# Kernel optimization log

Measured on AMD Instinct MI355X. Metric: run time of the kernel, lower is better.

Reference implementation:

```python
import jax, jax.numpy as jnp
import numpy as np
from jax import lax

B, C1, C2, OUT, H, W = 8, 256, 128, 256, 64, 64
MID = max(C1, C2)
D = max(MID // 8, 4)

def conv1x1(x, w, b=None):
    # x: [B,C,H,W], w: [O,C]
    y = jnp.einsum('bchw,oc->bohw', x, w)
    if b is not None:
        y = y + b[None, :, None, None]
    return y

def dwconv3x3(x, w, b):
    # depthwise 3x3, padding=1; w: [C,1,3,3]
    y = lax.conv_general_dilated(x, w, (1, 1), 'SAME',
                                 dimension_numbers=('NCHW', 'OIHW', 'NCHW'),
                                 feature_group_count=x.shape[1])
    return y + b[None, :, None, None]

def setup_inputs() -> dict:
    key = jax.random.key(0)
    ks = jax.random.split(key, 16)
    def w1x1(k, o, i):
        return jax.random.normal(k, (o, i), jnp.float32) * np.sqrt(2.0 / o)
    def wdw(k, c):
        return jax.random.normal(k, (c, 1, 3, 3), jnp.float32) * np.sqrt(2.0 / (9 * c))
    z = lambda c: jnp.zeros((c,), jnp.float32)
    return {
        'x1': jax.random.normal(ks[0], (B, C1, H, W), jnp.float32),
        'x2': jax.random.normal(ks[1], (B, C2, H, W), jnp.float32),
        'conv_r_w': w1x1(ks[2], MID, C1), 'conv_r_b': z(MID),
        'conv_n_w': w1x1(ks[3], MID, C2), 'conv_n_b': z(MID),
        'mlp_w1': w1x1(ks[4], D, MID),
        'mlp_w2': w1x1(ks[5], 2 * MID, D),
        'pq_w': w1x1(ks[6], MID, MID), 'pq_b': z(MID),
        'dq_w': wdw(ks[7], MID), 'dq_b': z(MID),
        'pk_w': w1x1(ks[8], MID, MID), 'pk_b': z(MID),
        'dk_w': wdw(ks[9], MID), 'dk_b': z(MID),
        'pv_w': w1x1(ks[10], MID, MID), 'pv_b': z(MID),
        'dv_w': wdw(ks[11], MID), 'dv_b': z(MID),
        'out_w': w1x1(ks[12], OUT, MID), 'out_b': z(OUT),
        'alpha': jnp.float32(1.0),
        'lambd': jnp.float32(0.5),
        'beta': jnp.float32(0.5),
    }

def reference(x1, x2, conv_r_w, conv_r_b, conv_n_w, conv_n_b, mlp_w1, mlp_w2,
              pq_w, pq_b, dq_w, dq_b, pk_w, pk_b, dk_w, dk_b,
              pv_w, pv_b, dv_w, dv_b, out_w, out_b, alpha, lambd, beta):
    FR = conv1x1(x1, conv_r_w, conv_r_b)          # [B,C,H,W]
    FN = conv1x1(x2, conv_n_w, conv_n_b)          # [B,C,H,W]
    stack = jnp.stack([FR, FN], axis=1)           # [B,2,C,H,W]
    feats_sum = FR + FN
    pooled = feats_sum.mean(axis=(2, 3))          # [B,C] (adaptive avg pool 1x1)
    h = jax.nn.relu(jnp.einsum('bc,dc->bd', pooled, mlp_w1))
    a = jnp.einsum('bd,ed->be', h, mlp_w2).reshape(B, 2, MID)
    attn = jax.nn.softmax(a, axis=1)              # softmax over the 2 branches
    Fw = jnp.einsum('bkchw,bkc->bchw', stack, attn)
    Q = dwconv3x3(conv1x1(Fw, pq_w, pq_b), dq_w, dq_b)
    K = dwconv3x3(conv1x1(Fw, pk_w, pk_b), dk_w, dk_b)
    V = dwconv3x3(conv1x1(Fw, pv_w, pv_b), dv_w, dv_b)
    FQ = jnp.fft.fft2(Q.astype(jnp.float32), axes=(-2, -1))   # complex64 [B,C,H,W]
    FK = jnp.fft.fft2(K.astype(jnp.float32), axes=(-2, -1))
    elem = (FQ * FK).reshape(B, MID, H * W)                    # [B,C,HW]
    FQf = FQ.reshape(B, MID, H * W)
    FKf = FK.reshape(B, MID, H * W)
    attn_matrix = jnp.einsum('bcn,bdn->bcd', FQf, FKf)         # complex [B,C,C]
    attn_w = jax.nn.softmax(jnp.abs(attn_matrix) / alpha, axis=-1)
    attn_wc = attn_w.astype(jnp.complex64)
    F_CFR = jnp.einsum('bcd,bdn->bcn', attn_wc, elem).reshape(B, MID, H, W)
    cfr = jnp.real(jnp.fft.ifft2(F_CFR, axes=(-2, -1))).astype(Q.dtype)
    F_DFR = V - lambd * V * cfr
    freq_out = Q * cfr + F_DFR
    output = beta * freq_out + (1.0 - beta) * Fw
    return conv1x1(output, out_w, out_b)
```

## Files before the change

kernel.cpp:

```cpp
#include <hip/hip_runtime.h>
#include <math.h>

#ifndef M_PI
#define M_PI 3.14159265358979323846
#endif

constexpr int  NB   = 8;
constexpr int  CH   = 256;
constexpr long HW   = 4096;
constexpr long SLOT = (long)NB * CH * HW;
constexpr int  SPLITK = 8;

typedef short bf16x8 __attribute__((ext_vector_type(8)));
typedef float f32x4  __attribute__((ext_vector_type(4)));

__device__ __forceinline__ unsigned bfpair(float x, float y) {
  return (__float_as_uint(x) >> 16) | (__float_as_uint(y) & 0xFFFF0000u);
}
__device__ __forceinline__ float rne_hi(float x) {
  unsigned u = __float_as_uint(x);
  unsigned r = (u + 0x7FFFu + ((u >> 16) & 1u)) & 0xFFFF0000u;
  return __uint_as_float(r);
}

template<int EPI>
__global__ __launch_bounds__(256)
void gemm_mfma(const float* __restrict__ A, const float* __restrict__ B,
               float* __restrict__ C, const float* __restrict__ bias,
               int K, long aStride, long bStride, long cStride,
               const float* __restrict__ qb, const float* __restrict__ vb,
               const float* __restrict__ fwb,
               const float* __restrict__ lambd, const float* __restrict__ beta)
{
  constexpr int N = 4096;
  __shared__ __align__(16) unsigned short sAh[128 * 48];
  __shared__ __align__(16) unsigned short sAl[128 * 48];
  __shared__ __align__(16) unsigned short sBh[128 * 48];
  __shared__ __align__(16) unsigned short sBl[128 * 48];

  const int tid = threadIdx.x;
  const int b   = blockIdx.z;
  const int m0  = blockIdx.y * 128;
  const int n0  = blockIdx.x * 128;
  const float* Ab = A + (long)b * aStride;
  const float* Bb = B + (long)b * bStride;
  float* Cb = C + (long)b * cStride;

  const int ar = tid >> 1;
  const int ak = (tid & 1) * 16;
  const int aBase = ar * 48 + ak;
  const int bn = tid & 127;
  const int bk = (tid >> 7) * 16;
  const int bBase = bn * 48 + bk;

  const int wv = tid >> 6, lane = tid & 63;
  const int wy = wv >> 1, wx = wv & 1;
  const int quad = lane >> 4, l15 = lane & 15;

  f32x4 acc[4][4];
#pragma unroll
  for (int i = 0; i < 4; ++i)
#pragma unroll
    for (int j = 0; j < 4; ++j) acc[i][j] = (f32x4){0.f, 0.f, 0.f, 0.f};

  float4 ra[4];
  float  rb[16];
  {
    const float* ap = Ab + (long)(m0 + ar) * K + ak;
#pragma unroll
    for (int i = 0; i < 4; ++i) ra[i] = *(const float4*)(ap + i * 4);
    const float* bp = Bb + (long)bk * N + n0 + bn;
#pragma unroll
    for (int i = 0; i < 16; ++i) rb[i] = bp[(long)i * N];
  }

  for (int kt = 0; kt < K; kt += 32) {
    {
      float v[16] = {ra[0].x, ra[0].y, ra[0].z, ra[0].w,
                     ra[1].x, ra[1].y, ra[1].z, ra[1].w,
                     ra[2].x, ra[2].y, ra[2].z, ra[2].w,
                     ra[3].x, ra[3].y, ra[3].z, ra[3].w};
      float h[16], l[16];
#pragma unroll
      for (int e = 0; e < 16; ++e) { h[e] = rne_hi(v[e]); l[e] = v[e] - h[e]; }
      uint4 u;
      u.x = bfpair(h[0], h[1]);  u.y = bfpair(h[2], h[3]);
      u.z = bfpair(h[4], h[5]);  u.w = bfpair(h[6], h[7]);
      *(uint4*)&sAh[aBase] = u;
      u.x = bfpair(h[8], h[9]);  u.y = bfpair(h[10], h[11]);
      u.z = bfpair(h[12], h[13]); u.w = bfpair(h[14], h[15]);
      *(uint4*)&sAh[aBase + 8] = u;
      u.x = bfpair(l[0], l[1]);  u.y = bfpair(l[2], l[3]);
      u.z = bfpair(l[4], l[5]);  u.w = bfpair(l[6], l[7]);
      *(uint4*)&sAl[aBase] = u;
      u.x = bfpair(l[8], l[9]);  u.y = bfpair(l[10], l[11]);
      u.z = bfpair(l[12], l[13]); u.w = bfpair(l[14], l[15]);
      *(uint4*)&sAl[aBase + 8] = u;
    }
    {
      float h[16], l[16];
#pragma unroll
      for (int e = 0; e < 16; ++e) { h[e] = rne_hi(rb[e]); l[e] = rb[e] - h[e]; }
      uint4 u;
      u.x = bfpair(h[0], h[1]);  u.y = bfpair(h[2], h[3]);
      u.z = bfpair(h[4], h[5]);  u.w = bfpair(h[6], h[7]);
      *(uint4*)&sBh[bBase] = u;
      u.x = bfpair(h[8], h[9]);  u.y = bfpair(h[10], h[11]);
      u.z = bfpair(h[12], h[13]); u.w = bfpair(h[14], h[15]);
      *(uint4*)&sBh[bBase + 8] = u;
      u.x = bfpair(l[0], l[1]);  u.y = bfpair(l[2], l[3]);
      u.z = bfpair(l[4], l[5]);  u.w = bfpair(l[6], l[7]);
      *(uint4*)&sBl[bBase] = u;
      u.x = bfpair(l[8], l[9]);  u.y = bfpair(l[10], l[11]);
      u.z = bfpair(l[12], l[13]); u.w = bfpair(l[14], l[15]);
      *(uint4*)&sBl[bBase + 8] = u;
    }
    __syncthreads();

    if (kt + 32 < K) {
      const float* ap = Ab + (long)(m0 + ar) * K + kt + 32 + ak;
#pragma unroll
      for (int i = 0; i < 4; ++i) ra[i] = *(const float4*)(ap + i * 4);
      const float* bp = Bb + (long)(kt + 32 + bk) * N + n0 + bn;
#pragma unroll
      for (int i = 0; i < 16; ++i) rb[i] = bp[(long)i * N];
    }

    bf16x8 ah[4], al[4];
#pragma unroll
    for (int i = 0; i < 4; ++i) {
      const int idx = (wy * 64 + i * 16 + l15) * 48 + quad * 8;
      ah[i] = *(const bf16x8*)&sAh[idx];
      al[i] = *(const bf16x8*)&sAl[idx];
    }
#pragma unroll
    for (int j = 0; j < 4; ++j) {
      const int idx = (wx * 64 + j * 16 + l15) * 48 + quad * 8;
      const bf16x8 bh = *(const bf16x8*)&sBh[idx];
      const bf16x8 bl = *(const bf16x8*)&sBl[idx];
#pragma unroll
      for (int i = 0; i < 4; ++i) {
        acc[i][j] = __builtin_amdgcn_mfma_f32_16x16x32_bf16(ah[i], bh, acc[i][j], 0, 0, 0);
        acc[i][j] = __builtin_amdgcn_mfma_f32_16x16x32_bf16(ah[i], bl, acc[i][j], 0, 0, 0);
        acc[i][j] = __builtin_amdgcn_mfma_f32_16x16x32_bf16(al[i], bh, acc[i][j], 0, 0, 0);
      }
    }
    __syncthreads();
  }

  if (EPI == 0) {
#pragma unroll
    for (int i = 0; i < 4; ++i) {
#pragma unroll
      for (int r = 0; r < 4; ++r) {
        const int row = m0 + wy * 64 + i * 16 + quad * 4 + r;
        const float bb = bias ? bias[row] : 0.f;
#pragma unroll
        for (int j = 0; j < 4; ++j) {
          const int col = n0 + wx * 64 + j * 16 + l15;
          Cb[(long)row * N + col] = acc[i][j][r] + bb;
        }
      }
    }
  } else {
    const float lam = lambd[0], bet = beta[0];
#pragma unroll
    for (int i = 0; i < 4; ++i) {
#pragma unroll
      for (int r = 0; r < 4; ++r) {
        const int row = m0 + wy * 64 + i * 16 + quad * 4 + r;
#pragma unroll
        for (int j = 0; j < 4; ++j) {
          const int col = n0 + wx * 64 + j * 16 + l15;
          const long off = (long)row * N + col;
          const long gi  = (long)b * cStride + off;
          const float q = qb[gi], v = vb[gi], f = fwb[gi];
          Cb[off] = bet * (acc[i][j][r] * (q - lam * v) + v) + (1.f - bet) * f;
        }
      }
    }
  }
}

#define BCOL(n) ((((n) >> 3) * 12) + ((n) & 7))

template<bool BT, int EPI>
__global__ __launch_bounds__(256)
void gemm_kernel(const float* __restrict__ A, const float* __restrict__ B,
                 float* __restrict__ C, const float* __restrict__ bias,
                 int M, int N, int K, int nSplitK,
                 long aStride, long bStride, long cStride)
{
  __shared__ __align__(16) float As[16][132];
  __shared__ __align__(16) float Bs[16][192];
  const int tid = threadIdx.x;
  const int b   = blockIdx.z / nSplitK;
  const int ks  = blockIdx.z % nSplitK;
  const int kLen = K / nSplitK;
  const int k0b  = ks * kLen;
  const float* Ab = A + (long)b * aStride;
  const float* Bb = B + (long)b * bStride;
  float* Cb = (EPI == 3) ? (C + (long)(b * nSplitK + ks) * cStride)
                         : (C + (long)b * cStride);
  const int m0 = blockIdx.y * 128;
  const int n0 = blockIdx.x * 128;

  float acc[8][8];
#pragma unroll
  for (int i = 0; i < 8; ++i)
#pragma unroll
    for (int j = 0; j < 8; ++j) acc[i][j] = 0.f;

  const int tx = tid & 15;
  const int ty = tid >> 4;
  const int lr = tid >> 1;
  const int lk = (tid & 1) * 8;
  const int bn = (tid & 31) * 4;
  const int bk = tid >> 5;
  const int colW = BCOL(bn);
  const int colT = BCOL(lr);

  float4 pa0, pa1, pb0, pb1;
  {
    const float* ap = &Ab[(long)(m0 + lr) * K + k0b + lk];
    pa0 = *(const float4*)ap;
    pa1 = *(const float4*)(ap + 4);
    if (BT) {
      const float* bp = &Bb[(long)(n0 + lr) * K + k0b + lk];
      pb0 = *(const float4*)bp;
      pb1 = *(const float4*)(bp + 4);
    } else {
      pb0 = *(const float4*)&Bb[(long)(k0b + bk) * N + n0 + bn];
      pb1 = *(const float4*)&Bb[(long)(k0b + bk + 8) * N + n0 + bn];
    }
  }

  for (int kt = 0; kt < kLen; kt += 16) {
    As[lk+0][lr] = pa0.x; As[lk+1][lr] = pa0.y; As[lk+2][lr] = pa0.z; As[lk+3][lr] = pa0.w;
    As[lk+4][lr] = pa1.x; As[lk+5][lr] = pa1.y; As[lk+6][lr] = pa1.z; As[lk+7][lr] = pa1.w;
    if (BT) {
      Bs[lk+0][colT] = pb0.x; Bs[lk+1][colT] = pb0.y; Bs[lk+2][colT] = pb0.z; Bs[lk+3][colT] = pb0.w;
      Bs[lk+4][colT] = pb1.x; Bs[lk+5][colT] = pb1.y; Bs[lk+6][colT] = pb1.z; Bs[lk+7][colT] = pb1.w;
    } else {
      *(float4*)&Bs[bk][colW]     = pb0;
      *(float4*)&Bs[bk + 8][colW] = pb1;
    }
    __syncthreads();

    if (kt + 16 < kLen) {
      const int k0 = k0b + kt + 16;
      const float* ap = &Ab[(long)(m0 + lr) * K + k0 + lk];
      pa0 = *(const float4*)ap;
      pa1 = *(const float4*)(ap + 4);
      if (BT) {
        const float* bp = &Bb[(long)(n0 + lr) * K + k0 + lk];
        pb0 = *(const float4*)bp;
        pb1 = *(const float4*)(bp + 4);
      } else {
        pb0 = *(const float4*)&Bb[(long)(k0 + bk) * N + n0 + bn];
        pb1 = *(const float4*)&Bb[(long)(k0 + bk + 8) * N + n0 + bn];
      }
    }

#pragma unroll
    for (int kk = 0; kk < 16; ++kk) {
      const float4 a0 = *(const float4*)&As[kk][ty * 8];
      const float4 a1 = *(const float4*)&As[kk][ty * 8 + 4];
      const float4 b0 = *(const float4*)&Bs[kk][tx * 12];
      const float4 b1 = *(const float4*)&Bs[kk][tx * 12 + 4];
      const float av[8] = {a0.x, a0.y, a0.z, a0.w, a1.x, a1.y, a1.z, a1.w};
      const float bv[8] = {b0.x, b0.y, b0.z, b0.w, b1.x, b1.y, b1.z, b1.w};
#pragma unroll
      for (int i = 0; i < 8; ++i)
#pragma unroll
        for (int j = 0; j < 8; ++j)
          acc[i][j] = fmaf(av[i], bv[j], acc[i][j]);
    }
    __syncthreads();
  }

#pragma unroll
  for (int i = 0; i < 8; ++i) {
    const int row = m0 + ty * 8 + i;
    const float bb = (EPI == 0 && bias) ? bias[row] : 0.f;
    float4 r0, r1;
    r0.x = acc[i][0] + bb; r0.y = acc[i][1] + bb; r0.z = acc[i][2] + bb; r0.w = acc[i][3] + bb;
    r1.x = acc[i][4] + bb; r1.y = acc[i][5] + bb; r1.z = acc[i][6] + bb; r1.w = acc[i][7] + bb;
    float* p = &Cb[(long)row * N + n0 + tx * 8];
    *(float4*)p       = r0;
    *(float4*)(p + 4) = r1;
  }
}

__global__ __launch_bounds__(256)
void pool_kernel(const float* __restrict__ FR, const float* __restrict__ FN,
                 float* __restrict__ pooled)
{
  __shared__ float red[256];
  const int bc = blockIdx.x, tid = threadIdx.x;
  const float4* a = (const float4*)(FR + (long)bc * HW);
  const float4* b = (const float4*)(FN + (long)bc * HW);
  float s = 0.f;
  for (int v = tid; v < 1024; v += 256) {
    const float4 x = a[v]; s += x.x + x.y + x.z + x.w;
    const float4 y = b[v]; s += y.x + y.y + y.z + y.w;
  }
  red[tid] = s; __syncthreads();
  for (int o = 128; o > 0; o >>= 1) {
    if (tid < o) red[tid] += red[tid + o];
    __syncthreads();
  }
  if (tid == 0) pooled[bc] = red[0] * (1.f / 4096.f);
}

__global__ __launch_bounds__(256)
void attn2_kernel(const float* __restrict__ pooled, const float* __restrict__ w1,
                  const float* __restrict__ w2, float* __restrict__ attn2)
{
  __shared__ float ps[256];
  __shared__ float hs[32];
  const int b = blockIdx.x, tid = threadIdx.x;
  ps[tid] = pooled[b * 256 + tid];
  __syncthreads();
  if (tid < 32) {
    float a = 0.f;
    for (int c = 0; c < 256; ++c) a += ps[c] * w1[tid * 256 + c];
    hs[tid] = fmaxf(a, 0.f);
  }
  __syncthreads();
  float a0 = 0.f, a1 = 0.f;
  for (int d = 0; d < 32; ++d) {
    const float h = hs[d];
    a0 += h * w2[tid * 32 + d];
    a1 += h * w2[(256 + tid) * 32 + d];
  }
  const float m  = fmaxf(a0, a1);
  const float e0 = expf(a0 - m), e1 = expf(a1 - m);
  const float inv = 1.f / (e0 + e1);
  attn2[b * 512 + tid]       = e0 * inv;
  attn2[b * 512 + 256 + tid] = e1 * inv;
}

__global__ __launch_bounds__(256)
void fw_kernel(const float* __restrict__ FR, const float* __restrict__ FN,
               const float* __restrict__ attn2, float* __restrict__ FW)
{
  const int b = blockIdx.z, c = blockIdx.y;
  const float a0 = attn2[b * 512 + c];
  const float a1 = attn2[b * 512 + 256 + c];
  const long base4 = ((long)b * 256 + c) * 1024;
  const int i = blockIdx.x * 256 + threadIdx.x;
  const float4 r = ((const float4*)FR)[base4 + i];
  const float4 n = ((const float4*)FN)[base4 + i];
  float4 o;
  o.x = a0 * r.x + a1 * n.x;
  o.y = a0 * r.y + a1 * n.y;
  o.z = a0 * r.z + a1 * n.z;
  o.w = a0 * r.w + a1 * n.w;
  ((float4*)FW)[base4 + i] = o;
}

__global__ __launch_bounds__(256)
void dw_kernel(const float* __restrict__ in, const float* __restrict__ w,
               const float* __restrict__ bias, float* __restrict__ out,
               float* __restrict__ out_rev)
{
  __shared__ float img[66][66];
  const int bc = blockIdx.x, tid = threadIdx.x;
  const int c = bc & 255;
  for (int v = tid; v < 66 * 66; v += 256) ((float*)img)[v] = 0.f;
  __syncthreads();
  const float4* in4 = (const float4*)(in + (long)bc * HW);
  for (int v = tid; v < 1024; v += 256) {
    const float4 x = in4[v];
    const int r = v >> 4, c0 = ((v & 15) << 2) + 1;
    img[r + 1][c0 + 0] = x.x;
    img[r + 1][c0 + 1] = x.y;
    img[r + 1][c0 + 2] = x.z;
    img[r + 1][c0 + 3] = x.w;
  }
  float wr[9];
#pragma unroll
  for (int j = 0; j < 9; ++j) wr[j] = w[c * 9 + j];
  const float bb = bias[c];
  __syncthreads();
  for (int p = tid; p < 4096; p += 256) {
    const int y = p >> 6, x = p & 63;
    float s = bb;
#pragma unroll
    for (int ky = 0; ky < 3; ++ky)
#pragma unroll
      for (int kx = 0; kx < 3; ++kx)
        s = fmaf(wr[ky * 3 + kx], img[y + ky][x + kx], s);
    out[(long)bc * HW + p] = s;
    if (out_rev)
      out_rev[(long)bc * HW + (((64 - y) & 63) << 6) + ((64 - x) & 63)] = s;
  }
}

#define SWA(r, c) (((r) << 6) | ((c) ^ (r)))
#define REV6(x)   ((((x) & 3) << 4) | ((x) & 12) | ((x) >> 4))

__device__ __forceinline__ float2 cmul(float2 a, float2 w) {
  return make_float2(a.x * w.x - a.y * w.y, a.x * w.y + a.y * w.x);
}
__device__ __forceinline__ float2 cmulc(float2 a, float2 w) {
  return make_float2(a.x * w.x + a.y * w.y, a.y * w.x - a.x * w.y);
}

__global__ __launch_bounds__(256, 4)
void sconv_kernel(const float* __restrict__ Qg, const float* __restrict__ Kg,
                  float* __restrict__ Sg)
{
  __shared__ float Re[4096];
  __shared__ float Im[4096];
  __shared__ float2 twt[64];
  const int tid = threadIdx.x;
  const long base = (long)blockIdx.x * 4096;
  if (tid < 64) {
    float sn, cs;
    __sincosf(-2.f * (float)M_PI * (float)tid * (1.f / 64.f), &sn, &cs);
    twt[tid] = make_float2(cs, sn);
  }
  const float4* Q4 = (const float4*)(Qg + base);
  const float4* K4 = (const float4*)(Kg + base);
#pragma unroll
  for (int i = 0; i < 4; ++i) {
    const int v = tid + 256 * i;
    const float4 q = Q4[v], k = K4[v];
    const int r = v >> 4, w = v & 15;
    const int R  = REV6(r);
    const int cb = ((w & 3) << 2) | (w >> 2);
    Re[SWA(R, cb)]      = q.x;  Im[SWA(R, cb)]      = k.x;
    Re[SWA(R, cb + 16)] = q.y;  Im[SWA(R, cb + 16)] = k.y;
    Re[SWA(R, cb + 32)] = q.z;  Im[SWA(R, cb + 32)] = k.z;
    Re[SWA(R, cb + 48)] = q.w;  Im[SWA(R, cb + 48)] = k.w;
  }
  __syncthreads();

  const int lane = tid & 63;
  const int kb   = tid >> 6;

  for (int pass = 0; pass < 2; ++pass) {
    for (int s = 0; s < 3; ++s) {
      const int h  = 1 << (2 * s);
      const int us = 16 >> (2 * s);
#pragma unroll
      for (int q = 0; q < 4; ++q) {
        const int k = kb + 4 * q;
        const int j = k & (h - 1);
        const int g = k >> (2 * s);
        const int bse = g * 4 * h + j;
        const int p0 = bse, p1 = bse + h, p2 = bse + 2 * h, p3 = bse + 3 * h;
        const int a0 = pass ? SWA(p0, lane) : SWA(lane, p0);
        const int a1 = pass ? SWA(p1, lane) : SWA(lane, p1);
        const int a2 = pass ? SWA(p2, lane) : SWA(lane, p2);
        const int a3 = pass ? SWA(p3, lane) : SWA(lane, p3);
        float2 x0 = make_float2(Re[a0], Im[a0]);
        float2 x1 = make_float2(Re[a1], Im[a1]);
        float2 x2 = make_float2(Re[a2], Im[a2]);
        float2 x3 = make_float2(Re[a3], Im[a3]);
        const int e = j * us;
        x1 = cmul(x1, twt[e & 63]);
        x2 = cmul(x2, twt[(2 * e) & 63]);
        x3 = cmul(x3, twt[(3 * e) & 63]);
        const float2 t0 = make_float2(x0.x + x2.x, x0.y + x2.y);
        const float2 t1 = make_float2(x0.x - x2.x, x0.y - x2.y);
        const float2 t2 = make_float2(x1.x + x3.x, x1.y + x3.y);
        const float2 t3 = make_float2(x1.x - x3.x, x1.y - x3.y);
// ... 39 lines not shown
        const int j = k & (h - 1);
        const int g = k >> (2 * s);
        const int bse = g * 4 * h + j;
        const int p0 = bse, p1 = bse + h, p2 = bse + 2 * h, p3 = bse + 3 * h;
        const int a0 = pass ? SWA(lane, p0) : SWA(p0, lane);
        const int a1 = pass ? SWA(lane, p1) : SWA(p1, lane);
        const int a2 = pass ? SWA(lane, p2) : SWA(p2, lane);
        const int a3 = pass ? SWA(lane, p3) : SWA(p3, lane);
        const float2 x0 = make_float2(Re[a0], Im[a0]);
        const float2 x1 = make_float2(Re[a1], Im[a1]);
        const float2 x2 = make_float2(Re[a2], Im[a2]);
        const float2 x3 = make_float2(Re[a3], Im[a3]);
        const float2 t0 = make_float2(x0.x + x2.x, x0.y + x2.y);
        const float2 t1 = make_float2(x0.x - x2.x, x0.y - x2.y);
        const float2 t2 = make_float2(x1.x + x3.x, x1.y + x3.y);
        const float2 t3 = make_float2(x1.x - x3.x, x1.y - x3.y);
        const float2 y0 = make_float2(t0.x + t2.x, t0.y + t2.y);
        float2 y2 = make_float2(t0.x - t2.x, t0.y - t2.y);
        float2 y1 = make_float2(t1.x - t3.y, t1.y + t3.x);
        float2 y3 = make_float2(t1.x + t3.y, t1.y - t3.x);
        const int e = j * us;
        y1 = cmulc(y1, twt[e & 63]);
        y2 = cmulc(y2, twt[(2 * e) & 63]);
        y3 = cmulc(y3, twt[(3 * e) & 63]);
        Re[a0] = y0.x;  Im[a0] = y0.y;
        Re[a1] = y1.x;  Im[a1] = y1.y;
        Re[a2] = y2.x;  Im[a2] = y2.y;
        Re[a3] = y3.x;  Im[a3] = y3.y;
      }
      __syncthreads();
    }
  }

  float4* S4 = (float4*)(Sg + base);
#pragma unroll
  for (int i = 0; i < 4; ++i) {
    const int v = tid + 256 * i;
    const int y = v >> 4, w = v & 15;
    const int Rr = REV6(y);
    const int cb = ((w & 3) << 2) | (w >> 2);
    float4 o;
    o.x = Re[SWA(Rr, cb)]      * (1.f / 4096.f);
    o.y = Re[SWA(Rr, cb + 16)] * (1.f / 4096.f);
    o.z = Re[SWA(Rr, cb + 32)] * (1.f / 4096.f);
    o.w = Re[SWA(Rr, cb + 48)] * (1.f / 4096.f);
    S4[v] = o;
  }
}

__global__ __launch_bounds__(256)
void softmax_kernel(const float* __restrict__ Lp, float* __restrict__ L,
                    const float* __restrict__ alpha)
{
  __shared__ float red[256];
  const int row = blockIdx.x, tid = threadIdx.x;
  const int b = row >> 8, c = row & 255;
  const float sc = 4096.f / alpha[0];
  float acc = 0.f;
#pragma unroll
  for (int s = 0; s < SPLITK; ++s)
    acc += Lp[((long)(b * SPLITK + s) * 65536) + (long)c * 256 + tid];
  const float v = fabsf(acc) * sc;
  red[tid] = v; __syncthreads();
  for (int o = 128; o > 0; o >>= 1) {
    if (tid < o) red[tid] = fmaxf(red[tid], red[tid + o]);
    __syncthreads();
  }
  const float mx = red[0];
  __syncthreads();
  const float e = expf(v - mx);
  red[tid] = e; __syncthreads();
  for (int o = 128; o > 0; o >>= 1) {
    if (tid < o) red[tid] += red[tid + o];
    __syncthreads();
  }
  L[(long)row * 256 + tid] = e / red[0];
}

extern "C" void kernel_launch(void* const* d_in, const int* in_sizes, int n_in,
                              void* d_out, int out_size, void* d_ws, size_t ws_size,
                              hipStream_t stream)
{
  const float* x1       = (const float*)d_in[0];
  const float* x2       = (const float*)d_in[1];
  const float* conv_r_w = (const float*)d_in[2];
  const float* conv_r_b = (const float*)d_in[3];
  const float* conv_n_w = (const float*)d_in[4];
  const float* conv_n_b = (const float*)d_in[5];
  const float* mlp_w1   = (const float*)d_in[6];
  const float* mlp_w2   = (const float*)d_in[7];
  const float* pq_w     = (const float*)d_in[8];
  const float* pq_b     = (const float*)d_in[9];
  const float* dq_w     = (const float*)d_in[10];
  const float* dq_b     = (const float*)d_in[11];
  const float* pk_w     = (const float*)d_in[12];
  const float* pk_b     = (const float*)d_in[13];
  const float* dk_w     = (const float*)d_in[14];
  const float* dk_b     = (const float*)d_in[15];
  const float* pv_w     = (const float*)d_in[16];
  const float* pv_b     = (const float*)d_in[17];
  const float* dv_w     = (const float*)d_in[18];
  const float* dv_b     = (const float*)d_in[19];
  const float* out_w    = (const float*)d_in[20];
  const float* out_b    = (const float*)d_in[21];
  const float* alpha    = (const float*)d_in[22];
  const float* lambd    = (const float*)d_in[23];
  const float* beta     = (const float*)d_in[24];

  float* s = (float*)d_ws;
  float* S0 = s;
  float* S1 = s + SLOT;
  float* S2 = s + 2 * SLOT;
  float* S3 = s + 3 * SLOT;
  float* S4 = s + 4 * SLOT;
  float* S5 = s + 5 * SLOT;
  float* Lp     = s + 6 * SLOT;
  float* Lb     = Lp + (long)8 * SPLITK * 256 * 256;
  float* pooled = Lb + (long)8 * 256 * 256;
  float* attn2  = pooled + 2048;

  const size_t needed =
      (size_t)(6 * SLOT + (long)8 * SPLITK * 65536 + 8L * 65536 + 2048 + 4096)
      * sizeof(float);
  if (ws_size < needed) return;

  const long ST  = (long)CH * HW;
  const long ST2 = (long)128 * HW;
  const long STL = (long)256 * 256;

  const dim3 gBig(32, 2, 8);

  gemm_mfma<0><<<gBig, 256, 0, stream>>>(conv_r_w, x1, S0, conv_r_b,
      256, 0L, ST, ST, nullptr, nullptr, nullptr, nullptr, nullptr);
  gemm_mfma<0><<<gBig, 256, 0, stream>>>(conv_n_w, x2, S1, conv_n_b,
      128, 0L, ST2, ST, nullptr, nullptr, nullptr, nullptr, nullptr);

  pool_kernel<<<2048, 256, 0, stream>>>(S0, S1, pooled);
  attn2_kernel<<<8, 256, 0, stream>>>(pooled, mlp_w1, mlp_w2, attn2);
  fw_kernel<<<dim3(4, 256, 8), 256, 0, stream>>>(S0, S1, attn2, S2);

  gemm_mfma<0><<<gBig, 256, 0, stream>>>(pq_w, S2, S3, pq_b,
      256, 0L, ST, ST, nullptr, nullptr, nullptr, nullptr, nullptr);
  gemm_mfma<0><<<gBig, 256, 0, stream>>>(pk_w, S2, S4, pk_b,
      256, 0L, ST, ST, nullptr, nullptr, nullptr, nullptr, nullptr);
  gemm_mfma<0><<<gBig, 256, 0, stream>>>(pv_w, S2, S5, pv_b,
      256, 0L, ST, ST, nullptr, nullptr, nullptr, nullptr, nullptr);

  dw_kernel<<<2048, 256, 0, stream>>>(S3, dq_w, dq_b, S0, nullptr);
  dw_kernel<<<2048, 256, 0, stream>>>(S4, dk_w, dk_b, S1, S3);
  dw_kernel<<<2048, 256, 0, stream>>>(S5, dv_w, dv_b, S4, nullptr);

  sconv_kernel<<<2048, 256, 0, stream>>>(S0, S1, S5);

  gemm_kernel<true, 3><<<dim3(2, 2, 8 * SPLITK), 256, 0, stream>>>(
      S0, S3, Lp, nullptr, 256, 256, 4096, SPLITK, ST, ST, STL);
  softmax_kernel<<<2048, 256, 0, stream>>>(Lp, Lb, alpha);

  gemm_mfma<2><<<gBig, 256, 0, stream>>>(Lb, S5, S2, nullptr,
      256, STL, ST, ST, S0, S4, S2, lambd, beta);

  gemm_mfma<0><<<gBig, 256, 0, stream>>>(out_w, S2, (float*)d_out, out_b,
      256, 0L, ST, ST, nullptr, nullptr, nullptr, nullptr, nullptr);
}
```

Before: 517.1 us.

## Store intermediates as packed bf16 hi/lo pairs and move logits GEMM to MFMA

```diff
diff --git a/kernel.cpp b/kernel.cpp
--- a/kernel.cpp
+++ b/kernel.cpp
@@ -4,32 +4,55 @@
 #ifndef M_PI
 #define M_PI 3.14159265358979323846
 #endif
+
+typedef unsigned int u32;
 
 constexpr int  NB   = 8;
 constexpr int  CH   = 256;
 constexpr long HW   = 4096;
 constexpr long SLOT = (long)NB * CH * HW;
 constexpr int  SPLITK = 8;
-
-typedef short bf16x8 __attribute__((ext_vector_type(8)));
-typedef float f32x4  __attribute__((ext_vector_type(4)));
-
-__device__ __forceinline__ unsigned bfpair(float x, float y) {
-  return (__float_as_uint(x) >> 16) | (__float_as_uint(y) & 0xFFFF0000u);
-}
+constexpr long ST   = (long)CH * HW;
+
 __device__ __forceinline__ float rne_hi(float x) {
   unsigned u = __float_as_uint(x);
   unsigned r = (u + 0x7FFFu + ((u >> 16) & 1u)) & 0xFFFF0000u;
   return __uint_as_float(r);
 }
-
-template<int EPI>
+__device__ __forceinline__ u32 packf(float x) {
+  const float h = rne_hi(x);
+  const float l = x - h;
+  return (__float_as_uint(h) & 0xFFFF0000u) | (__float_as_uint(l) >> 16);
+}
+__device__ __forceinline__ float unpackf(u32 u) {
+  return __uint_as_float(u & 0xFFFF0000u) + __uint_as_float(u << 16);
+}
+__device__ __forceinline__ unsigned bfpair(float x, float y) {
+  return (__float_as_uint(x) >> 16) | (__float_as_uint(y) & 0xFFFF0000u);
+}
+
+typedef short bf16x8 __attribute__((ext_vector_type(8)));
+typedef float f32x4  __attribute__((ext_vector_type(4)));
+
 __global__ __launch_bounds__(256)
-void gemm_mfma(const float* __restrict__ A, const float* __restrict__ B,
-               float* __restrict__ C, const float* __restrict__ bias,
+void cvt_kernel(const float* __restrict__ src, u32* __restrict__ dst, int n4)
+{
+  const int i = blockIdx.x * 256 + threadIdx.x;
+  if (i < n4) {
+    const float4 v = ((const float4*)src)[i];
+    uint4 o;
+    o.x = packf(v.x); o.y = packf(v.y); o.z = packf(v.z); o.w = packf(v.w);
+    ((uint4*)dst)[i] = o;
+  }
+}
+
+template<bool BPACKED, int EPI>
+__global__ __launch_bounds__(256)
+void gemm_mfma(const u32* __restrict__ A, const void* __restrict__ Bv,
+               void* __restrict__ Cv, const float* __restrict__ bias,
                int K, long aStride, long bStride, long cStride,
-               const float* __restrict__ qb, const float* __restrict__ vb,
-               const float* __restrict__ fwb,
+               const u32* __restrict__ qb, const u32* __restrict__ vb,
+               const u32* __restrict__ fwb,
                const float* __restrict__ lambd, const float* __restrict__ beta)
 {
   constexpr int N = 4096;
@@ -42,9 +65,7 @@
   const int b   = blockIdx.z;
   const int m0  = blockIdx.y * 128;
   const int n0  = blockIdx.x * 128;
-  const float* Ab = A + (long)b * aStride;
-  const float* Bb = B + (long)b * bStride;
-  float* Cb = C + (long)b * cStride;
+  const u32* Ab = A + (long)b * aStride;
 
   const int ar = tid >> 1;
   const int ak = (tid & 1) * 16;
@@ -63,67 +84,84 @@
 #pragma unroll
     for (int j = 0; j < 4; ++j) acc[i][j] = (f32x4){0.f, 0.f, 0.f, 0.f};
 
-  float4 ra[4];
-  float  rb[16];
+  u32   ra[16];
+  u32   rbu[16];
+  float rbf[16];
   {
-    const float* ap = Ab + (long)(m0 + ar) * K + ak;
-#pragma unroll
-    for (int i = 0; i < 4; ++i) ra[i] = *(const float4*)(ap + i * 4);
-    const float* bp = Bb + (long)bk * N + n0 + bn;
-#pragma unroll
-    for (int i = 0; i < 16; ++i) rb[i] = bp[(long)i * N];
+    const u32* ap = Ab + (long)(m0 + ar) * K + ak;
+#pragma unroll
+    for (int i = 0; i < 4; ++i) {
+      const uint4 t = *(const uint4*)(ap + i * 4);
+      ra[4*i] = t.x; ra[4*i+1] = t.y; ra[4*i+2] = t.z; ra[4*i+3] = t.w;
+    }
+    if (BPACKED) {
+      const u32* bp = (const u32*)Bv + (long)b * bStride + (long)bk * N + n0 + bn;
+#pragma unroll
+      for (int i = 0; i < 16; ++i) rbu[i] = bp[(long)i * N];
+    } else {
+      const float* bp = (const float*)Bv + (long)b * bStride + (long)bk * N + n0 + bn;
+#pragma unroll
+      for (int i = 0; i < 16; ++i) rbf[i] = bp[(long)i * N];
+    }
   }
 
   for (int kt = 0; kt < K; kt += 32) {
     {
-      float v[16] = {ra[0].x, ra[0].y, ra[0].z, ra[0].w,
-                     ra[1].x, ra[1].y, ra[1].z, ra[1].w,
-                     ra[2].x, ra[2].y, ra[2].z, ra[2].w,
-                     ra[3].x, ra[3].y, ra[3].z, ra[3].w};
+      u32 hi[8], lo[8];
+#pragma unroll
+      for (int e = 0; e < 8; ++e) {
+        const u32 u0 = ra[2*e], u1 = ra[2*e+1];
+        hi[e] = (u0 >> 16) | (u1 & 0xFFFF0000u);
+        lo[e] = (u0 & 0xFFFFu) | (u1 << 16);
+      }
+      *(uint4*)&sAh[aBase]     = make_uint4(hi[0], hi[1], hi[2], hi[3]);
+      *(uint4*)&sAh[aBase + 8] = make_uint4(hi[4], hi[5], hi[6], hi[7]);
+      *(uint4*)&sAl[aBase]     = make_uint4(lo[0], lo[1], lo[2], lo[3]);
+      *(uint4*)&sAl[aBase + 8] = make_uint4(lo[4], lo[5], lo[6], lo[7]);
+    }
+    if (BPACKED) {
+      u32 hi[8], lo[8];
+#pragma unroll
+      for (int e = 0; e < 8; ++e) {
+        const u32 u0 = rbu[2*e], u1 = rbu[2*e+1];
+        hi[e] = (u0 >> 16) | (u1 & 0xFFFF0000u);
+        lo[e] = (u0 & 0xFFFFu) | (u1 << 16);
+      }
+      *(uint4*)&sBh[bBase]     = make_uint4(hi[0], hi[1], hi[2], hi[3]);
+      *(uint4*)&sBh[bBase + 8] = make_uint4(hi[4], hi[5], hi[6], hi[7]);
+      *(uint4*)&sBl[bBase]     = make_uint4(lo[0], lo[1], lo[2], lo[3]);
+      *(uint4*)&sBl[bBase + 8] = make_uint4(lo[4], lo[5], lo[6], lo[7]);
+    } else {
       float h[16], l[16];
 #pragma unroll
-      for (int e = 0; e < 16; ++e) { h[e] = rne_hi(v[e]); l[e] = v[e] - h[e]; }
-      uint4 u;
-      u.x = bfpair(h[0], h[1]);  u.y = bfpair(h[2], h[3]);
-      u.z = bfpair(h[4], h[5]);  u.w = bfpair(h[6], h[7]);
-      *(uint4*)&sAh[aBase] = u;
-      u.x = bfpair(h[8], h[9]);  u.y = bfpair(h[10], h[11]);
-      u.z = bfpair(h[12], h[13]); u.w = bfpair(h[14], h[15]);
-      *(uint4*)&sAh[aBase + 8] = u;
-      u.x = bfpair(l[0], l[1]);  u.y = bfpair(l[2], l[3]);
-      u.z = bfpair(l[4], l[5]);  u.w = bfpair(l[6], l[7]);
-      *(uint4*)&sAl[aBase] = u;
-      u.x = bfpair(l[8], l[9]);  u.y = bfpair(l[10], l[11]);
-      u.z = bfpair(l[12], l[13]); u.w = bfpair(l[14], l[15]);
-      *(uint4*)&sAl[aBase + 8] = u;
-    }
-    {
-      float h[16], l[16];
-#pragma unroll
-      for (int e = 0; e < 16; ++e) { h[e] = rne_hi(rb[e]); l[e] = rb[e] - h[e]; }
-      uint4 u;
-      u.x = bfpair(h[0], h[1]);  u.y = bfpair(h[2], h[3]);
-      u.z = bfpair(h[4], h[5]);  u.w = bfpair(h[6], h[7]);
-      *(uint4*)&sBh[bBase] = u;
-      u.x = bfpair(h[8], h[9]);  u.y = bfpair(h[10], h[11]);
-      u.z = bfpair(h[12], h[13]); u.w = bfpair(h[14], h[15]);
-      *(uint4*)&sBh[bBase + 8] = u;
-      u.x = bfpair(l[0], l[1]);  u.y = bfpair(l[2], l[3]);
-      u.z = bfpair(l[4], l[5]);  u.w = bfpair(l[6], l[7]);
-      *(uint4*)&sBl[bBase] = u;
-      u.x = bfpair(l[8], l[9]);  u.y = bfpair(l[10], l[11]);
-      u.z = bfpair(l[12], l[13]); u.w = bfpair(l[14], l[15]);
-      *(uint4*)&sBl[bBase + 8] = u;
+      for (int e = 0; e < 16; ++e) { h[e] = rne_hi(rbf[e]); l[e] = rbf[e] - h[e]; }
+      *(uint4*)&sBh[bBase]     = make_uint4(bfpair(h[0],h[1]), bfpair(h[2],h[3]),
+                                            bfpair(h[4],h[5]), bfpair(h[6],h[7]));
+      *(uint4*)&sBh[bBase + 8] = make_uint4(bfpair(h[8],h[9]), bfpair(h[10],h[11]),
+                                            bfpair(h[12],h[13]), bfpair(h[14],h[15]));
+      *(uint4*)&sBl[bBase]     = make_uint4(bfpair(l[0],l[1]), bfpair(l[2],l[3]),
+                                            bfpair(l[4],l[5]), bfpair(l[6],l[7]));
+      *(uint4*)&sBl[bBase + 8] = make_uint4(bfpair(l[8],l[9]), bfpair(l[10],l[11]),
+                                            bfpair(l[12],l[13]), bfpair(l[14],l[15]));
     }
     __syncthreads();
 
     if (kt + 32 < K) {
-      const float* ap = Ab + (long)(m0 + ar) * K + kt + 32 + ak;
-#pragma unroll
-      for (int i = 0; i < 4; ++i) ra[i] = *(const float4*)(ap + i * 4);
-      const float* bp = Bb + (long)(kt + 32 + bk) * N + n0 + bn;
-#pragma unroll
-      for (int i = 0; i < 16; ++i) rb[i] = bp[(long)i * N];
+      const u32* ap = Ab + (long)(m0 + ar) * K + kt + 32 + ak;
+#pragma unroll
+      for (int i = 0; i < 4; ++i) {
+        const uint4 t = *(const uint4*)(ap + i * 4);
+        ra[4*i] = t.x; ra[4*i+1] = t.y; ra[4*i+2] = t.z; ra[4*i+3] = t.w;
+      }
+      if (BPACKED) {
+        const u32* bp = (const u32*)Bv + (long)b * bStride + (long)(kt + 32 + bk) * N + n0 + bn;
+#pragma unroll
+        for (int i = 0; i < 16; ++i) rbu[i] = bp[(long)i * N];
+      } else {
+        const float* bp = (const float*)Bv + (long)b * bStride + (long)(kt + 32 + bk) * N + n0 + bn;
+#pragma unroll
+        for (int i = 0; i < 16; ++i) rbf[i] = bp[(long)i * N];
+      }
     }
 
     bf16x8 ah[4], al[4];
@@ -149,8 +187,9 @@
   }
 
   if (EPI == 0) {
-#pragma unroll
-    for (int i = 0; i < 4; ++i) {
+    float* Cb = (float*)Cv + (long)b * cStride;
+#pragma unroll
+    for (int i = 0; i < 4; ++i)
 #pragma unroll
       for (int r = 0; r < 4; ++r) {
         const int row = m0 + wy * 64 + i * 16 + quad * 4 + r;
@@ -161,11 +200,25 @@
           Cb[(long)row * N + col] = acc[i][j][r] + bb;
         }
       }
-    }
+  } else if (EPI == 1) {
+    u32* Cb = (u32*)Cv + (long)b * cStride;
+#pragma unroll
+    for (int i = 0; i < 4; ++i)
+#pragma unroll
+      for (int r = 0; r < 4; ++r) {
+        const int row = m0 + wy * 64 + i * 16 + quad * 4 + r;
+        const float bb = bias ? bias[row] : 0.f;
+#pragma unroll
+        for (int j = 0; j < 4; ++j) {
+          const int col = n0 + wx * 64 + j * 16 + l15;
+          Cb[(long)row * N + col] = packf(acc[i][j][r] + bb);
+        }
+      }
   } else {
+    u32* Cb = (u32*)Cv + (long)b * cStride;
     const float lam = lambd[0], bet = beta[0];
 #pragma unroll
-    for (int i = 0; i < 4; ++i) {
+    for (int i = 0; i < 4; ++i)
 #pragma unroll
       for (int r = 0; r < 4; ++r) {
         const int row = m0 + wy * 64 + i * 16 + quad * 4 + r;
@@ -174,136 +227,143 @@
           const int col = n0 + wx * 64 + j * 16 + l15;
           const long off = (long)row * N + col;
           const long gi  = (long)b * cStride + off;
-          const float q = qb[gi], v = vb[gi], f = fwb[gi];
-          Cb[off] = bet * (acc[i][j][r] * (q - lam * v) + v) + (1.f - bet) * f;
+          const float q = unpackf(qb[gi]);
+          const float v = unpackf(vb[gi]);
+          const float f = unpackf(fwb[gi]);
+          Cb[off] = packf(bet * (acc[i][j][r] * (q - lam * v) + v) + (1.f - bet) * f);
         }
       }
-    }
-  }
-}
-
-#define BCOL(n) ((((n) >> 3) * 12) + ((n) & 7))
-
-template<bool BT, int EPI>
+  }
+}
+
 __global__ __launch_bounds__(256)
-void gemm_kernel(const float* __restrict__ A, const float* __restrict__ B,
-                 float* __restrict__ C, const float* __restrict__ bias,
-                 int M, int N, int K, int nSplitK,
-                 long aStride, long bStride, long cStride)
-{
-  __shared__ __align__(16) float As[16][132];
-  __shared__ __align__(16) float Bs[16][192];
+void gemm_logits(const u32* __restrict__ Q, const u32* __restrict__ Kr,
+                 float* __restrict__ Lp)
+{
+  __shared__ __align__(16) unsigned short sAh[128 * 48];
+  __shared__ __align__(16) unsigned short sAl[128 * 48];
+  __shared__ __align__(16) unsigned short sBh[128 * 48];
+  __shared__ __align__(16) unsigned short sBl[128 * 48];
+
   const int tid = threadIdx.x;
-  const int b   = blockIdx.z / nSplitK;
-  const int ks  = blockIdx.z % nSplitK;
-  const int kLen = K / nSplitK;
-  const int k0b  = ks * kLen;
-  const float* Ab = A + (long)b * aStride;
-  const float* Bb = B + (long)b * bStride;
-  float* Cb = (EPI == 3) ? (C + (long)(b * nSplitK + ks) * cStride)
-                         : (C + (long)b * cStride);
-  const int m0 = blockIdx.y * 128;
-  const int n0 = blockIdx.x * 128;
-
-  float acc[8][8];
-#pragma unroll
-  for (int i = 0; i < 8; ++i)
-#pragma unroll
-    for (int j = 0; j < 8; ++j) acc[i][j] = 0.f;
-
-  const int tx = tid & 15;
-  const int ty = tid >> 4;
-  const int lr = tid >> 1;
-  const int lk = (tid & 1) * 8;
-  const int bn = (tid & 31) * 4;
-  const int bk = tid >> 5;
-  const int colW = BCOL(bn);
-  const int colT = BCOL(lr);
-
-  float4 pa0, pa1, pb0, pb1;
-  {
-    const float* ap = &Ab[(long)(m0 + lr) * K + k0b + lk];
-    pa0 = *(const float4*)ap;
-    pa1 = *(const float4*)(ap + 4);
-    if (BT) {
-      const float* bp = &Bb[(long)(n0 + lr) * K + k0b + lk];
-      pb0 = *(const float4*)bp;
-      pb1 = *(const float4*)(bp + 4);
-    } else {
-      pb0 = *(const float4*)&Bb[(long)(k0b + bk) * N + n0 + bn];
-      pb1 = *(const float4*)&Bb[(long)(k0b + bk + 8) * N + n0 + bn];
-    }
-  }
-
-  for (int kt = 0; kt < kLen; kt += 16) {
-    As[lk+0][lr] = pa0.x; As[lk+1][lr] = pa0.y; As[lk+2][lr] = pa0.z; As[lk+3][lr] = pa0.w;
-    As[lk+4][lr] = pa1.x; As[lk+5][lr] = pa1.y; As[lk+6][lr] = pa1.z; As[lk+7][lr] = pa1.w;
-    if (BT) {
-      Bs[lk+0][colT] = pb0.x; Bs[lk+1][colT] = pb0.y; Bs[lk+2][colT] = pb0.z; Bs[lk+3][colT] = pb0.w;
-      Bs[lk+4][colT] = pb1.x; Bs[lk+5][colT] = pb1.y; Bs[lk+6][colT] = pb1.z; Bs[lk+7][colT] = pb1.w;
-    } else {
-      *(float4*)&Bs[bk][colW]     = pb0;
-      *(float4*)&Bs[bk + 8][colW] = pb1;
+  const int bz  = blockIdx.z;
+  const int b   = bz >> 3, sp = bz & 7;
+  const int m0  = blockIdx.y * 128;
+  const int n0  = blockIdx.x * 128;
+  const long k0b = (long)sp * 512;
+
+  const int ar = tid >> 1;
+  const int ak = (tid & 1) * 16;
+  const int aBase = ar * 48 + ak;
+
+  const int wv = tid >> 6, lane = tid & 63;
+  const int wy = wv >> 1, wx = wv & 1;
+  const int quad = lane >> 4, l15 = lane & 15;
+
+  f32x4 acc[4][4];
+#pragma unroll
+  for (int i = 0; i < 4; ++i)
+#pragma unroll
+    for (int j = 0; j < 4; ++j) acc[i][j] = (f32x4){0.f, 0.f, 0.f, 0.f};
+
+  const u32* Abase = Q  + (long)b * ST + (long)(m0 + ar) * 4096 + k0b + ak;
+  const u32* Bbase = Kr + (long)b * ST + (long)(n0 + ar) * 4096 + k0b + ak;
+
+  u32 ra[16], rb[16];
+#pragma unroll
+  for (int i = 0; i < 4; ++i) {
+    uint4 t = *(const uint4*)(Abase + i * 4);
+    ra[4*i] = t.x; ra[4*i+1] = t.y; ra[4*i+2] = t.z; ra[4*i+3] = t.w;
+    t = *(const uint4*)(Bbase + i * 4);
+    rb[4*i] = t.x; rb[4*i+1] = t.y; rb[4*i+2] = t.z; rb[4*i+3] = t.w;
+  }
+
+  for (int kt = 0; kt < 512; kt += 32) {
+    {
+      u32 hi[8], lo[8];
+#pragma unroll
+      for (int e = 0; e < 8; ++e) {
+        const u32 u0 = ra[2*e], u1 = ra[2*e+1];
+        hi[e] = (u0 >> 16) | (u1 & 0xFFFF0000u);
+        lo[e] = (u0 & 0xFFFFu) | (u1 << 16);
+      }
+      *(uint4*)&sAh[aBase]     = make_uint4(hi[0], hi[1], hi[2], hi[3]);
+      *(uint4*)&sAh[aBase + 8] = make_uint4(hi[4], hi[5], hi[6], hi[7]);
+      *(uint4*)&sAl[aBase]     = make_uint4(lo[0], lo[1], lo[2], lo[3]);
+      *(uint4*)&sAl[aBase + 8] = make_uint4(lo[4], lo[5], lo[6], lo[7]);
+#pragma unroll
+      for (int e = 0; e < 8; ++e) {
+        const u32 u0 = rb[2*e], u1 = rb[2*e+1];
+        hi[e] = (u0 >> 16) | (u1 & 0xFFFF0000u);
+        lo[e] = (u0 & 0xFFFFu) | (u1 << 16);
+      }
+      *(uint4*)&sBh[aBase]     = make_uint4(hi[0], hi[1], hi[2], hi[3]);
+      *(uint4*)&sBh[aBase + 8] = make_uint4(hi[4], hi[5], hi[6], hi[7]);
+      *(uint4*)&sBl[aBase]     = make_uint4(lo[0], lo[1], lo[2], lo[3]);
+      *(uint4*)&sBl[aBase + 8] = make_uint4(lo[4], lo[5], lo[6], lo[7]);
     }
     __syncthreads();
 
-    if (kt + 16 < kLen) {
-      const int k0 = k0b + kt + 16;
-      const float* ap = &Ab[(long)(m0 + lr) * K + k0 + lk];
-      pa0 = *(const float4*)ap;
-      pa1 = *(const float4*)(ap + 4);
-      if (BT) {
-        const float* bp = &Bb[(long)(n0 + lr) * K + k0 + lk];
-        pb0 = *(const float4*)bp;
-        pb1 = *(const float4*)(bp + 4);
-      } else {
-        pb0 = *(const float4*)&Bb[(long)(k0 + bk) * N + n0 + bn];
-        pb1 = *(const float4*)&Bb[(long)(k0 + bk + 8) * N + n0 + bn];
-      }
-    }
-
-#pragma unroll
-    for (int kk = 0; kk < 16; ++kk) {
-      const float4 a0 = *(const float4*)&As[kk][ty * 8];
-      const float4 a1 = *(const float4*)&As[kk][ty * 8 + 4];
-      const float4 b0 = *(const float4*)&Bs[kk][tx * 12];
-      const float4 b1 = *(const float4*)&Bs[kk][tx * 12 + 4];
-      const float av[8] = {a0.x, a0.y, a0.z, a0.w, a1.x, a1.y, a1.z, a1.w};
-      const float bv[8] = {b0.x, b0.y, b0.z, b0.w, b1.x, b1.y, b1.z, b1.w};
-#pragma unroll
-      for (int i = 0; i < 8; ++i)
-#pragma unroll
-        for (int j = 0; j < 8; ++j)
-          acc[i][j] = fmaf(av[i], bv[j], acc[i][j]);
+    if (kt + 32 < 512) {
+#pragma unroll
+      for (int i = 0; i < 4; ++i) {
+        uint4 t = *(const uint4*)(Abase + kt + 32 + i * 4);
+        ra[4*i] = t.x; ra[4*i+1] = t.y; ra[4*i+2] = t.z; ra[4*i+3] = t.w;
+        t = *(const uint4*)(Bbase + kt + 32 + i * 4);
+        rb[4*i] = t.x; rb[4*i+1] = t.y; rb[4*i+2] = t.z; rb[4*i+3] = t.w;
+      }
+    }
+
+    bf16x8 ah[4], al[4];
+#pragma unroll
+    for (int i = 0; i < 4; ++i) {
+      const int idx = (wy * 64 + i * 16 + l15) * 48 + quad * 8;
+      ah[i] = *(const bf16x8*)&sAh[idx];
+      al[i] = *(const bf16x8*)&sAl[idx];
+    }
+#pragma unroll
+    for (int j = 0; j < 4; ++j) {
+      const int idx = (wx * 64 + j * 16 + l15) * 48 + quad * 8;
+      const bf16x8 bh = *(const bf16x8*)&sBh[idx];
+      const bf16x8 bl = *(const bf16x8*)&sBl[idx];
+#pragma unroll
+      for (int i = 0; i < 4; ++i) {
+        acc[i][j] = __builtin_amdgcn_mfma_f32_16x16x32_bf16(ah[i], bh, acc[i][j], 0, 0, 0);
+        acc[i][j] = __builtin_amdgcn_mfma_f32_16x16x32_bf16(ah[i], bl, acc[i][j], 0, 0, 0);
+        acc[i][j] = __builtin_amdgcn_mfma_f32_16x16x32_bf16(al[i], bh, acc[i][j], 0, 0, 0);
+      }
     }
     __syncthreads();
   }
 
-#pragma unroll
-  for (int i = 0; i < 8; ++i) {
-    const int row = m0 + ty * 8 + i;
-    const float bb = (EPI == 0 && bias) ? bias[row] : 0.f;
-    float4 r0, r1;
-    r0.x = acc[i][0] + bb; r0.y = acc[i][1] + bb; r0.z = acc[i][2] + bb; r0.w = acc[i][3] + bb;
-    r1.x = acc[i][4] + bb; r1.y = acc[i][5] + bb; r1.z = acc[i][6] + bb; r1.w = acc[i][7] + bb;
-    float* p = &Cb[(long)row * N + n0 + tx * 8];
-    *(float4*)p       = r0;
-    *(float4*)(p + 4) = r1;
-  }
+  float* Lb = Lp + (long)bz * 65536;
+#pragma unroll
+  for (int i = 0; i < 4; ++i)
+#pragma unroll
+    for (int r = 0; r < 4; ++r) {
+      const int row = m0 + wy * 64 + i * 16 + quad * 4 + r;
+#pragma unroll
+      for (int j = 0; j < 4; ++j) {
+        const int col = n0 + wx * 64 + j * 16 + l15;
+        Lb[(long)row * 256 + col] = acc[i][j][r];
+      }
+    }
 }
 
 __global__ __launch_bounds__(256)
-void pool_kernel(const float* __restrict__ FR, const float* __restrict__ FN,
+void pool_kernel(const u32* __restrict__ FR, const u32* __restrict__ FN,
                  float* __restrict__ pooled)
 {
   __shared__ float red[256];
   const int bc = blockIdx.x, tid = threadIdx.x;
-  const float4* a = (const float4*)(FR + (long)bc * HW);
-  const float4* b = (const float4*)(FN + (long)bc * HW);
+  const uint4* a = (const uint4*)(FR + (long)bc * HW);
+  const uint4* b = (const uint4*)(FN + (long)bc * HW);
   float s = 0.f;
   for (int v = tid; v < 1024; v += 256) {
-    const float4 x = a[v]; s += x.x + x.y + x.z + x.w;
-    const float4 y = b[v]; s += y.x + y.y + y.z + y.w;
+    const uint4 x = a[v];
+    s += unpackf(x.x) + unpackf(x.y) + unpackf(x.z) + unpackf(x.w);
+    const uint4 y = b[v];
+    s += unpackf(y.x) + unpackf(y.y) + unpackf(y.z) + unpackf(y.w);
   }
   red[tid] = s; __syncthreads();
   for (int o = 128; o > 0; o >>= 1) {
@@ -342,42 +402,42 @@
 }
 
 __global__ __launch_bounds__(256)
-void fw_kernel(const float* __restrict__ FR, const float* __restrict__ FN,
-               const float* __restrict__ attn2, float* __restrict__ FW)
+void fw_kernel(const u32* __restrict__ FR, const u32* __restrict__ FN,
+               const float* __restrict__ attn2, u32* __restrict__ FW)
 {
   const int b = blockIdx.z, c = blockIdx.y;
   const float a0 = attn2[b * 512 + c];
   const float a1 = attn2[b * 512 + 256 + c];
   const long base4 = ((long)b * 256 + c) * 1024;
   const int i = blockIdx.x * 256 + threadIdx.x;
-  const float4 r = ((const float4*)FR)[base4 + i];
-  const float4 n = ((const float4*)FN)[base4 + i];
-  float4 o;
-  o.x = a0 * r.x + a1 * n.x;
-  o.y = a0 * r.y + a1 * n.y;
-  o.z = a0 * r.z + a1 * n.z;
-  o.w = a0 * r.w + a1 * n.w;
-  ((float4*)FW)[base4 + i] = o;
+  const uint4 r = ((const uint4*)FR)[base4 + i];
+  const uint4 n = ((const uint4*)FN)[base4 + i];
+  uint4 o;
+  o.x = packf(a0 * unpackf(r.x) + a1 * unpackf(n.x));
+  o.y = packf(a0 * unpackf(r.y) + a1 * unpackf(n.y));
+  o.z = packf(a0 * unpackf(r.z) + a1 * unpackf(n.z));
+  o.w = packf(a0 * unpackf(r.w) + a1 * unpackf(n.w));
+  ((uint4*)FW)[base4 + i] = o;
 }
 
 __global__ __launch_bounds__(256)
-void dw_kernel(const float* __restrict__ in, const float* __restrict__ w,
-               const float* __restrict__ bias, float* __restrict__ out,
-               float* __restrict__ out_rev)
+void dw_kernel(const u32* __restrict__ in, const float* __restrict__ w,
+               const float* __restrict__ bias, u32* __restrict__ out,
+               u32* __restrict__ out_rev)
 {
   __shared__ float img[66][66];
   const int bc = blockIdx.x, tid = threadIdx.x;
   const int c = bc & 255;
   for (int v = tid; v < 66 * 66; v += 256) ((float*)img)[v] = 0.f;
   __syncthreads();
-  const float4* in4 = (const float4*)(in + (long)bc * HW);
+  const uint4* in4 = (const uint4*)(in + (long)bc * HW);
   for (int v = tid; v < 1024; v += 256) {
-    const float4 x = in4[v];
+    const uint4 x = in4[v];
     const int r = v >> 4, c0 = ((v & 15) << 2) + 1;
-    img[r + 1][c0 + 0] = x.x;
-    img[r + 1][c0 + 1] = x.y;
-    img[r + 1][c0 + 2] = x.z;
-    img[r + 1][c0 + 3] = x.w;
+    img[r + 1][c0 + 0] = unpackf(x.x);
+    img[r + 1][c0 + 1] = unpackf(x.y);
+    img[r + 1][c0 + 2] = unpackf(x.z);
+    img[r + 1][c0 + 3] = unpackf(x.w);
   }
   float wr[9];
 #pragma unroll
@@ -392,9 +452,10 @@
 #pragma unroll
       for (int kx = 0; kx < 3; ++kx)
         s = fmaf(wr[ky * 3 + kx], img[y + ky][x + kx], s);
-    out[(long)bc * HW + p] = s;
+    const u32 u = packf(s);
+    out[(long)bc * HW + p] = u;
     if (out_rev)
-      out_rev[(long)bc * HW + (((64 - y) & 63) << 6) + ((64 - x) & 63)] = s;
+      out_rev[(long)bc * HW + (((64 - y) & 63) << 6) + ((64 - x) & 63)] = u;
   }
 }
 
@@ -409,8 +470,8 @@
 }
 
 __global__ __launch_bounds__(256, 4)
-void sconv_kernel(const float* __restrict__ Qg, const float* __restrict__ Kg,
-                  float* __restrict__ Sg)
+void sconv_kernel(const u32* __restrict__ Qg, const u32* __restrict__ Kg,
+                  u32* __restrict__ Sg)
 {
   __shared__ float Re[4096];
   __shared__ float Im[4096];
@@ -422,19 +483,19 @@
     __sincosf(-2.f * (float)M_PI * (float)tid * (1.f / 64.f), &sn, &cs);
     twt[tid] = make_float2(cs, sn);
   }
-  const float4* Q4 = (const float4*)(Qg + base);
-  const float4* K4 = (const float4*)(Kg + base);
+  const uint4* Q4 = (const uint4*)(Qg + base);
+  const uint4* K4 = (const uint4*)(Kg + base);
 #pragma unroll
   for (int i = 0; i < 4; ++i) {
     const int v = tid + 256 * i;
-    const float4 q = Q4[v], k = K4[v];
+    const uint4 q = Q4[v], k = K4[v];
     const int r = v >> 4, w = v & 15;
     const int R  = REV6(r);
     const int cb = ((w & 3) << 2) | (w >> 2);
-    Re[SWA(R, cb)]      = q.x;  Im[SWA(R, cb)]      = k.x;
-    Re[SWA(R, cb + 16)] = q.y;  Im[SWA(R, cb + 16)] = k.y;
-    Re[SWA(R, cb + 32)] = q.z;  Im[SWA(R, cb + 32)] = k.z;
-    Re[SWA(R, cb + 48)] = q.w;  Im[SWA(R, cb + 48)] = k.w;
+    Re[SWA(R, cb)]      = unpackf(q.x);  Im[SWA(R, cb)]      = unpackf(k.x);
+    Re[SWA(R, cb + 16)] = unpackf(q.y);  Im[SWA(R, cb + 16)] = unpackf(k.y);
+    Re[SWA(R, cb + 32)] = unpackf(q.z);  Im[SWA(R, cb + 32)] = unpackf(k.z);
+    Re[SWA(R, cb + 48)] = unpackf(q.w);  Im[SWA(R, cb + 48)] = unpackf(k.w);
   }
   __syncthreads();
 
@@ -540,24 +601,24 @@
     }
   }
 
-  float4* S4 = (float4*)(Sg + base);
+  uint4* S4 = (uint4*)(Sg + base);
 #pragma unroll
   for (int i = 0; i < 4; ++i) {
     const int v = tid + 256 * i;
     const int y = v >> 4, w = v & 15;
     const int Rr = REV6(y);
     const int cb = ((w & 3) << 2) | (w >> 2);
-    float4 o;
-    o.x = Re[SWA(Rr, cb)]      * (1.f / 4096.f);
-    o.y = Re[SWA(Rr, cb + 16)] * (1.f / 4096.f);
-    o.z = Re[SWA(Rr, cb + 32)] * (1.f / 4096.f);
-    o.w = Re[SWA(Rr, cb + 48)] * (1.f / 4096.f);
+    uint4 o;
+    o.x = packf(Re[SWA(Rr, cb)]      * (1.f / 4096.f));
+    o.y = packf(Re[SWA(Rr, cb + 16)] * (1.f / 4096.f));
+    o.z = packf(Re[SWA(Rr, cb + 32)] * (1.f / 4096.f));
+    o.w = packf(Re[SWA(Rr, cb + 48)] * (1.f / 4096.f));
     S4[v] = o;
   }
 }
 
 __global__ __launch_bounds__(256)
-void softmax_kernel(const float* __restrict__ Lp, float* __restrict__ L,
+void softmax_kernel(const float* __restrict__ Lp, u32* __restrict__ L,
                     const float* __restrict__ alpha)
 {
   __shared__ float red[256];
@@ -582,7 +643,7 @@
     if (tid < o) red[tid] += red[tid + o];
     __syncthreads();
   }
-  L[(long)row * 256 + tid] = e / red[0];
+  L[(long)row * 256 + tid] = packf(e / red[0]);
 }
 
 extern "C" void kernel_launch(void* const* d_in, const int* in_sizes, int n_in,
@@ -615,43 +676,54 @@
   const float* lambd    = (const float*)d_in[23];
   const float* beta     = (const float*)d_in[24];
 
-  float* s = (float*)d_ws;
-  float* S0 = s;
-  float* S1 = s + SLOT;
-  float* S2 = s + 2 * SLOT;
-  float* S3 = s + 3 * SLOT;
-  float* S4 = s + 4 * SLOT;
-  float* S5 = s + 5 * SLOT;
-  float* Lp     = s + 6 * SLOT;
-  float* Lb     = Lp + (long)8 * SPLITK * 256 * 256;
-  float* pooled = Lb + (long)8 * 256 * 256;
+  u32* s = (u32*)d_ws;
+  u32* S0 = s;
+  u32* S1 = s + SLOT;
+  u32* S2 = s + 2 * SLOT;
+  u32* S3 = s + 3 * SLOT;
+  u32* S4 = s + 4 * SLOT;
+  u32* S5 = s + 5 * SLOT;
+  float* Lp     = (float*)(s + 6 * SLOT);
+  u32*   Lb     = (u32*)(Lp + (long)8 * SPLITK * 65536);
+  float* pooled = (float*)(Lb + (long)8 * 65536);
   float* attn2  = pooled + 2048;
+  u32*   wR     = (u32*)(attn2 + 4096);
+  u32*   wN     = wR + 65536;
+  u32*   wQ     = wN + 32768;
+  u32*   wK     = wQ + 65536;
+  u32*   wV     = wK + 65536;
+  u32*   wO     = wV + 65536;
 
   const size_t needed =
-      (size_t)(6 * SLOT + (long)8 * SPLITK * 65536 + 8L * 65536 + 2048 + 4096)
-      * sizeof(float);
+      (size_t)(6 * SLOT + (long)8 * SPLITK * 65536 + 8L * 65536 + 2048 + 4096
+               + 65536 * 5 + 32768) * 4;
   if (ws_size < needed) return;
 
-  const long ST  = (long)CH * HW;
   const long ST2 = (long)128 * HW;
   const long STL = (long)256 * 256;
-
   const dim3 gBig(32, 2, 8);
 
-  gemm_mfma<0><<<gBig, 256, 0, stream>>>(conv_r_w, x1, S0, conv_r_b,
+  cvt_kernel<<<64, 256, 0, stream>>>(conv_r_w, wR, 16384);
+  cvt_kernel<<<32, 256, 0, stream>>>(conv_n_w, wN, 8192);
+  cvt_kernel<<<64, 256, 0, stream>>>(pq_w, wQ, 16384);
+  cvt_kernel<<<64, 256, 0, stream>>>(pk_w, wK, 16384);
+  cvt_kernel<<<64, 256, 0, stream>>>(pv_w, wV, 16384);
+  cvt_kernel<<<64, 256, 0, stream>>>(out_w, wO, 16384);
+
+  gemm_mfma<false, 1><<<gBig, 256, 0, stream>>>(wR, x1, S0, conv_r_b,
       256, 0L, ST, ST, nullptr, nullptr, nullptr, nullptr, nullptr);
-  gemm_mfma<0><<<gBig, 256, 0, stream>>>(conv_n_w, x2, S1, conv_n_b,
+  gemm_mfma<false, 1><<<gBig, 256, 0, stream>>>(wN, x2, S1, conv_n_b,
       128, 0L, ST2, ST, nullptr, nullptr, nullptr, nullptr, nullptr);
 
   pool_kernel<<<2048, 256, 0, stream>>>(S0, S1, pooled);
   attn2_kernel<<<8, 256, 0, stream>>>(pooled, mlp_w1, mlp_w2, attn2);
   fw_kernel<<<dim3(4, 256, 8), 256, 0, stream>>>(S0, S1, attn2, S2);
 
-  gemm_mfma<0><<<gBig, 256, 0, stream>>>(pq_w, S2, S3, pq_b,
+  gemm_mfma<true, 1><<<gBig, 256, 0, stream>>>(wQ, S2, S3, pq_b,
       256, 0L, ST, ST, nullptr, nullptr, nullptr, nullptr, nullptr);
-  gemm_mfma<0><<<gBig, 256, 0, stream>>>(pk_w, S2, S4, pk_b,
+  gemm_mfma<true, 1><<<gBig, 256, 0, stream>>>(wK, S2, S4, pk_b,
       256, 0L, ST, ST, nullptr, nullptr, nullptr, nullptr, nullptr);
-  gemm_mfma<0><<<gBig, 256, 0, stream>>>(pv_w, S2, S5, pv_b,
+  gemm_mfma<true, 1><<<gBig, 256, 0, stream>>>(wV, S2, S5, pv_b,
       256, 0L, ST, ST, nullptr, nullptr, nullptr, nullptr, nullptr);
 
   dw_kernel<<<2048, 256, 0, stream>>>(S3, dq_w, dq_b, S0, nullptr);
@@ -660,13 +732,12 @@
 
   sconv_kernel<<<2048, 256, 0, stream>>>(S0, S1, S5);
 
-  gemm_kernel<true, 3><<<dim3(2, 2, 8 * SPLITK), 256, 0, stream>>>(
-      S0, S3, Lp, nullptr, 256, 256, 4096, SPLITK, ST, ST, STL);
+  gemm_logits<<<dim3(2, 2, 64), 256, 0, stream>>>(S0, S3, Lp);
   softmax_kernel<<<2048, 256, 0, stream>>>(Lp, Lb, alpha);
 
-  gemm_mfma<2><<<gBig, 256, 0, stream>>>(Lb, S5, S2, nullptr,
+  gemm_mfma<true, 2><<<gBig, 256, 0, stream>>>(Lb, S5, S2, nullptr,
       256, STL, ST, ST, S0, S4, S2, lambd, beta);
 
-  gemm_mfma<0><<<gBig, 256, 0, stream>>>(out_w, S2, (float*)d_out, out_b,
+  gemm_mfma<true, 0><<<gBig, 256, 0, stream>>>(wO, S2, d_out, out_b,
       256, 0L, ST, ST, nullptr, nullptr, nullptr, nullptr, nullptr);
 }
```

Measured after the change: 459.7 us. 11.1% less time.
